# Performance work log

Measured on AMD Instinct MI355X. Metric: run time of the kernel, lower is better.

The kernel has to match this reference:

```python
import jax, jax.numpy as jnp
import numpy as np


def _qkernel(r, i, j, k):
    # Build the real-valued block kernel of a quaternion dense layer.
    # r,i,j,k: [in/4, out/4] -> kernel [in, out] implementing the Hamilton product.
    col_r = jnp.concatenate([r, -i, -j, -k], axis=0)
    col_i = jnp.concatenate([i, r, -k, j], axis=0)
    col_j = jnp.concatenate([j, k, r, -i], axis=0)
    col_k = jnp.concatenate([k, -j, i, r], axis=0)
    return jnp.concatenate([col_r, col_i, col_j, col_k], axis=1)


def setup_inputs() -> dict:
    key = jax.random.key(0)
    ks = jax.random.split(key, 12)
    B, F, H = 32768, 1024, 256
    F4, H4 = F // 4, H // 4
    s_in = 1.0 / np.sqrt(F)
    s_h = 1.0 / np.sqrt(H)
    inp = {
        "x": jax.random.normal(ks[0], (B, F), dtype=jnp.float32),
        "wx_r": jax.random.normal(ks[1], (4, F4, H4), dtype=jnp.float32) * s_in,
        "wx_i": jax.random.normal(ks[2], (4, F4, H4), dtype=jnp.float32) * s_in,
        "wx_j": jax.random.normal(ks[3], (4, F4, H4), dtype=jnp.float32) * s_in,
        "wx_k": jax.random.normal(ks[4], (4, F4, H4), dtype=jnp.float32) * s_in,
        "bx": jnp.zeros((4, H), dtype=jnp.float32),
        "uh_r": jax.random.normal(ks[5], (4, H4, H4), dtype=jnp.float32) * s_h,
        "uh_i": jax.random.normal(ks[6], (4, H4, H4), dtype=jnp.float32) * s_h,
        "uh_j": jax.random.normal(ks[7], (4, H4, H4), dtype=jnp.float32) * s_h,
        "uh_k": jax.random.normal(ks[8], (4, H4, H4), dtype=jnp.float32) * s_h,
        "fco_w": jax.random.normal(ks[9], (H, H), dtype=jnp.float32) * s_h,
        "fco_b": jnp.zeros((H,), dtype=jnp.float32),
    }
    return inp


def reference(x, wx_r, wx_i, wx_j, wx_k, bx, uh_r, uh_i, uh_j, uh_k, fco_w, fco_b):
    # Single-step quaternion LSTM cell with zero initial hidden/cell state.
    # Gate order along leading axis: [forget, input, output, cell].
    Kx = jax.vmap(_qkernel)(wx_r, wx_i, wx_j, wx_k)   # [4, F, H]
    Ku = jax.vmap(_qkernel)(uh_r, uh_i, uh_j, uh_k)   # [4, H, H]
    H = bx.shape[1]
    h0 = jnp.zeros((x.shape[0], H), dtype=x.dtype)
    c0 = h0
    gx = jnp.einsum('bf,gfh->gbh', x, Kx) + bx[:, None, :]   # [4, B, H]
    gu = jnp.einsum('bh,ghk->gbk', h0, Ku)                    # [4, B, H]
    z = gx + gu
    ft = jax.nn.sigmoid(z[0])
    it = jax.nn.sigmoid(z[1])
    ot = jax.nn.sigmoid(z[2])
    at = z[3]
    c = it * jnp.tanh(at) + ft * c0
    h = ot * jnp.tanh(c)
    return h @ fco_w + fco_b
```

## Files before the change

kernel.cpp:

```cpp
#include <hip/hip_runtime.h>
#include <cstdint>
#include <cstddef>

#define WS_WP   0
#define WS_FCO  1572864
#define WS_BP   1703936
#define WS_HVP  1707008

typedef __attribute__((ext_vector_type(8))) __bf16 bf16x8;
typedef __attribute__((ext_vector_type(4))) __bf16 bf16x4;
typedef __attribute__((ext_vector_type(4))) float floatx4;

__device__ __forceinline__ unsigned short f2bf(float f) {
  unsigned int u = __builtin_bit_cast(unsigned int, f);
  u += 0x7fffu + ((u >> 16) & 1u);
  return (unsigned short)(u >> 16);
}

__device__ __forceinline__ float sigmf(float z) {
  return __builtin_amdgcn_rcpf(1.f + __expf(-z));
}
__device__ __forceinline__ float tanh_(float z) {
  return 1.f - 2.f * __builtin_amdgcn_rcpf(1.f + __expf(2.f * z));
}

__device__ __forceinline__ void gld16(const void* g, void* l) {
  __builtin_amdgcn_global_load_lds(
      (const __attribute__((address_space(1))) unsigned int*)g,
      (__attribute__((address_space(3))) unsigned int*)l, 16, 0, 0);
}

__global__ __launch_bounds__(256) void pack_k(
    const float* __restrict__ wr, const float* __restrict__ wi,
    const float* __restrict__ wj, const float* __restrict__ wk,
    const float* __restrict__ bx, const float* __restrict__ fw,
    unsigned short* __restrict__ Wp, unsigned short* __restrict__ Fp,
    float* __restrict__ bp) {
  int t = threadIdx.x;
  if (blockIdx.x < 384) {
    int gpp = blockIdx.x >> 7;
    int oct = blockIdx.x & 127;
    int gp = gpp + 1;
    int h = t;
    int hb = h >> 6, hr = h & 63;
    int f0 = oct << 3;
    int fb = f0 >> 8, fr0 = f0 & 255;
    const int   comp_t[4][4] = {{0,1,2,3},{1,0,3,2},{2,3,0,1},{3,2,1,0}};
    const float sign_t[4][4] = {{1.f,-1.f,-1.f,-1.f},{1.f,1.f,-1.f,1.f},
                                {1.f,1.f,1.f,-1.f},{1.f,-1.f,1.f,1.f}};
    const float* srcs[4] = {wr, wi, wj, wk};
    const float* s = srcs[comp_t[hb][fb]] + ((size_t)((gp << 8) + fr0)) * 64 + hr;
    float sg = sign_t[hb][fb];
    unsigned short v[8];
#pragma unroll
    for (int j = 0; j < 8; ++j) v[j] = f2bf(sg * s[(size_t)j * 64]);
    int c = h * 3 + gpp;
    int cb = c / 192, nl = c % 192;
    int kb = oct >> 2, q = oct & 3;
    int idx16 = (nl << 2) + (q ^ ((nl >> 1) & 3));
    uint4 val = make_uint4(
        (unsigned)v[0] | ((unsigned)v[1] << 16), (unsigned)v[2] | ((unsigned)v[3] << 16),
        (unsigned)v[4] | ((unsigned)v[5] << 16), (unsigned)v[6] | ((unsigned)v[7] << 16));
    *(uint4*)(Wp + (size_t)(cb * 32 + kb) * 6144 + idx16 * 8) = val;
    if (oct == 0) bp[c] = bx[(gp << 8) + h];
  } else {
    int oct = blockIdx.x - 384;
    int n = t;
    int k0 = oct << 3;
    unsigned short v[8];
#pragma unroll
    for (int j = 0; j < 8; ++j) v[j] = f2bf(fw[(size_t)(k0 + j) * 256 + n]);
    int nb = n >> 7, nl = n & 127, kb = oct >> 2, q = oct & 3;
    int idx16 = (nl << 2) + (q ^ ((nl >> 1) & 3));
    uint4 val = make_uint4(
        (unsigned)v[0] | ((unsigned)v[1] << 16), (unsigned)v[2] | ((unsigned)v[3] << 16),
        (unsigned)v[4] | ((unsigned)v[5] << 16), (unsigned)v[6] | ((unsigned)v[7] << 16));
    *(uint4*)(Fp + (size_t)((nb << 3) + kb) * 4096 + idx16 * 8) = val;
  }
}

__global__ __launch_bounds__(512, 4) void gemm1_k(
    const float* __restrict__ x, const unsigned short* __restrict__ Wp,
    const float* __restrict__ bp, unsigned short* __restrict__ hvp) {
  __shared__ char smem[57344];
  float* zep = (float*)smem;

  const int t = threadIdx.x;
  const int lane = t & 63, wid = t >> 6;
  const int wm = wid >> 2, wn = wid & 3;
  const int lrow = lane & 15, q = lane >> 4;
  const int rowt = blockIdx.x;
  const int nbq = blockIdx.y;
  const int cb0 = nbq * 2;
  const int row0 = rowt * 64;
  const float* xbase = x + (size_t)row0 * 1024;

  const int sr = t >> 3, kq = t & 7;
  const int sq8 = kq >> 1, shalf = kq & 1;

  floatx4 acc[2][6];
#pragma unroll
  for (int i = 0; i < 2; ++i)
#pragma unroll
    for (int j = 0; j < 6; ++j) acc[i][j] = (floatx4){0.f, 0.f, 0.f, 0.f};

#define STAGE_B(bufi, kt)                                                     \
  {                                                                           \
    unsigned short* sBs_ = (unsigned short*)(smem + (bufi) * 28672 + 4096);   \
    const unsigned short* bt0_ = Wp + ((size_t)cb0 * 32 + (kt)) * 6144;       \
    _Pragma("unroll")                                                         \
    for (int i_ = 0; i_ < 3; ++i_) {                                          \
      int s_ = t + i_ * 512;                                                  \
      int cbL_ = s_ >= 768;                                                   \
      const unsigned short* src_ =                                            \
          bt0_ + (size_t)cbL_ * 196608 + (s_ - cbL_ * 768) * 8;               \
      gld16(src_, sBs_ + s_ * 8);                                             \
    }                                                                         \
  }
#define LOAD_A(ra, kt)                                                        \
  { ra = *(const float4*)(xbase + (size_t)sr * 1024 + (kt) * 32 + kq * 4); }
#define WRITE_A(ra, bufi)                                                     \
  {                                                                           \
    unsigned short* sAs_ = (unsigned short*)(smem + (bufi) * 28672);          \
    int slot_ = (sr << 2) + (sq8 ^ ((sr >> 1) & 3));                          \
    bf16x4 v_;                                                                \
    v_[0] = (__bf16)ra.x; v_[1] = (__bf16)ra.y;                               \
    v_[2] = (__bf16)ra.z; v_[3] = (__bf16)ra.w;                               \
    *(bf16x4*)(sAs_ + slot_ * 8 + shalf * 4) = v_;                            \
  }
#define COMPUTE(bufi)                                                         \
  {                                                                           \
    const unsigned short* sA_ = (const unsigned short*)(smem + (bufi) * 28672);\
    const unsigned short* sB_ = sA_ + 2048;                                   \
    bf16x8 af[2], bf[6];                                                      \
    _Pragma("unroll")                                                         \
    for (int mt = 0; mt < 2; ++mt) {                                          \
      int m = wm * 32 + mt * 16 + lrow;                                       \
      int slot = (m << 2) + (q ^ ((m >> 1) & 3));                             \
      af[mt] = *(const bf16x8*)(const void*)(sA_ + slot * 8);                 \
    }                                                                         \
    _Pragma("unroll")                                                         \
    for (int nt = 0; nt < 6; ++nt) {                                          \
      int nl = (wn & 1) * 96 + nt * 16 + lrow;                                \
      int off16 = (nl << 2) + (q ^ ((nl >> 1) & 3));                          \
      bf[nt] = *(const bf16x8*)(const void*)(                                 \
          sB_ + ((size_t)(wn >> 1) * 768 + off16) * 8);                       \
    }                                                                         \
    _Pragma("unroll")                                                         \
    for (int mt = 0; mt < 2; ++mt)                                            \
      _Pragma("unroll")                                                       \
      for (int nt = 0; nt < 6; ++nt)                                          \
        acc[mt][nt] = __builtin_amdgcn_mfma_f32_16x16x32_bf16(                \
            af[mt], bf[nt], acc[mt][nt], 0, 0, 0);                            \
  }

  float4 ra;
  LOAD_A(ra, 0)
  STAGE_B(0, 0)
  WRITE_A(ra, 0)
  __syncthreads();

  for (int kt = 0; kt < 32; ++kt) {
    if (kt < 31) {
      LOAD_A(ra, kt + 1)
      STAGE_B((kt + 1) & 1, kt + 1)
    }
    COMPUTE(kt & 1)
    if (kt < 31) WRITE_A(ra, (kt + 1) & 1)
    __syncthreads();
  }
#undef COMPUTE
#undef STAGE_B
#undef LOAD_A
#undef WRITE_A

  const float* bp0 = bp + cb0 * 192;
  const int er = t >> 4, oc = t & 15;
  const int cbL = oc >> 3, oo = oc & 7;
  const int mb128 = rowt >> 1;
#pragma unroll
  for (int pass = 0; pass < 2; ++pass) {
    if (wm == pass) {
#pragma unroll
      for (int mt = 0; mt < 2; ++mt)
#pragma unroll
        for (int nt = 0; nt < 6; ++nt)
#pragma unroll
          for (int r = 0; r < 4; ++r)
            zep[(mt * 16 + q * 4 + r) * 385 + wn * 96 + nt * 16 + lrow] = acc[mt][nt][r];
    }
    __syncthreads();
    {
      int ml = (rowt & 1) * 64 + pass * 32 + er;
      unsigned short v[8];
#pragma unroll
      for (int j = 0; j < 8; ++j) {
        int hl = oo * 8 + j;
        int cz = cbL * 192 + hl * 3;
        float zi = zep[er * 385 + cz + 0] + bp0[cz + 0];
        float zo = zep[er * 385 + cz + 1] + bp0[cz + 1];
        float zc = zep[er * 385 + cz + 2] + bp0[cz + 2];
        float it = sigmf(zi);
        float ot = sigmf(zo);
        float cc = it * tanh_(zc);
        v[j] = f2bf(ot * tanh_(cc));
      }
      int ktile = (cb0 + cbL) * 2 + (oo >> 2), qq = oo & 3;
      int idx16 = (ml << 2) + (qq ^ ((ml >> 1) & 3));
      uint4 val = make_uint4(
          (unsigned)v[0] | ((unsigned)v[1] << 16), (unsigned)v[2] | ((unsigned)v[3] << 16),
          (unsigned)v[4] | ((unsigned)v[5] << 16), (unsigned)v[6] | ((unsigned)v[7] << 16));
      *(uint4*)(hvp + (size_t)(mb128 * 8 + ktile) * 4096 + idx16 * 8) = val;
    }
    __syncthreads();
  }
}

__global__ __launch_bounds__(256, 4) void gemm2_k(
    const unsigned short* __restrict__ hvp, const unsigned short* __restrict__ Fp,
    const float* __restrict__ fcob, float* __restrict__ out) {
  __shared__ unsigned short sB[32768];
  const int t = threadIdx.x;
  const int lane = t & 63, wid = t >> 6;
  const int wm = wid >> 1, wn = wid & 1;
  const int lrow = lane & 15, q = lane >> 4;
  const int mb = blockIdx.x, nb = blockIdx.y;

  const unsigned short* fpb = Fp + (size_t)nb * 32768;
#pragma unroll
  for (int i = 0; i < 16; ++i) gld16(fpb + (t + i * 256) * 8, sB + (t + i * 256) * 8);

  floatx4 acc[4][4];
#pragma unroll
  for (int i = 0; i < 4; ++i)
#pragma unroll
    for (int j = 0; j < 4; ++j) acc[i][j] = (floatx4){0.f, 0.f, 0.f, 0.f};
  __syncthreads();

#pragma unroll
  for (int kt = 0; kt < 8; ++kt) {
    const unsigned short* at_ = hvp + (size_t)(mb * 8 + kt) * 4096;
    bf16x8 af[4], bf[4];
#pragma unroll
    for (int mt = 0; mt < 4; ++mt) {
      int m = wm * 64 + mt * 16 + lrow;
      int o = (m << 2) + (q ^ ((m >> 1) & 3));
      af[mt] = *(const bf16x8*)(const void*)(at_ + o * 8);
    }
#pragma unroll
    for (int nt = 0; nt < 4; ++nt) {
      int n = wn * 64 + nt * 16 + lrow;
      int o = (n << 2) + (q ^ ((n >> 1) & 3));
      bf[nt] = *(const bf16x8*)(const void*)(sB + kt * 4096 + o * 8);
    }
#pragma unroll
    for (int mt = 0; mt < 4; ++mt)
#pragma unroll
      for (int nt = 0; nt < 4; ++nt)
        acc[mt][nt] = __builtin_amdgcn_mfma_f32_16x16x32_bf16(af[mt], bf[nt], acc[mt][nt], 0, 0, 0);
  }
#pragma unroll
  for (int nt = 0; nt < 4; ++nt) {
    int colg = nb * 128 + wn * 64 + nt * 16 + lrow;
    float bias = fcob[colg];
#pragma unroll
    for (int mt = 0; mt < 4; ++mt) {
      int rowg = mb * 128 + wm * 64 + mt * 16 + q * 4;
#pragma unroll
      for (int r = 0; r < 4; ++r)
        out[(size_t)(rowg + r) * 256 + colg] = acc[mt][nt][r] + bias;
    }
  }
}

extern "C" void kernel_launch(void* const* d_in, const int* in_sizes, int n_in,
                              void* d_out, int out_size, void* d_ws, size_t ws_size,
                              hipStream_t stream) {
  const float* x  = (const float*)d_in[0];
  const float* wr = (const float*)d_in[1];
  const float* wi = (const float*)d_in[2];
  const float* wj = (const float*)d_in[3];
  const float* wk = (const float*)d_in[4];
  const float* bx = (const float*)d_in[5];
  const float* fw = (const float*)d_in[10];
  const float* fb = (const float*)d_in[11];
  char* ws = (char*)d_ws;
  unsigned short* Wp  = (unsigned short*)(ws + WS_WP);
  unsigned short* Fp  = (unsigned short*)(ws + WS_FCO);
  float*          bp  = (float*)(ws + WS_BP);
  unsigned short* hvp = (unsigned short*)(ws + WS_HVP);
  float*          out = (float*)d_out;

  hipLaunchKernelGGL(pack_k,  dim3(416),    dim3(256), 0, stream, wr, wi, wj, wk, bx, fw, Wp, Fp, bp);
  hipLaunchKernelGGL(gemm1_k, dim3(512, 2), dim3(512), 0, stream, x, Wp, bp, hvp);
  hipLaunchKernelGGL(gemm2_k, dim3(256, 2), dim3(256), 0, stream, hvp, Fp, fb, out);
}
```

Baseline: 292.0 us.

## Pre-pack x into swizzled bf16 tiles and use async-LDS pipelined GEMM

Adds a pass to the packing kernel that converts the fp32 input x into bf16 tiles with an LDS-friendly swizzle in workspace. A new GEMM kernel streams those tiles with global_load_lds through a 3-stage buffer, using a 128x192 block tile and 256 threads. The aim is to halve GEMM operand bytes and remove in-loop conversion. The cost is an extra full read of x plus a bf16 write and re-read, and the path is used only when the workspace is large enough. Otherwise the old kernel runs.

New measurement: 298.9 us. 1.02x slower.

```diff
diff --git a/kernel.cpp b/kernel.cpp
--- a/kernel.cpp
+++ b/kernel.cpp
@@ -6,6 +6,8 @@
 #define WS_FCO  1572864
 #define WS_BP   1703936
 #define WS_HVP  1707008
+#define WS_XP   18484224
+#define WS_NEED 85593088ull
 
 typedef __attribute__((ext_vector_type(8))) __bf16 bf16x8;
 typedef __attribute__((ext_vector_type(4))) __bf16 bf16x4;
@@ -34,8 +36,9 @@
     const float* __restrict__ wr, const float* __restrict__ wi,
     const float* __restrict__ wj, const float* __restrict__ wk,
     const float* __restrict__ bx, const float* __restrict__ fw,
+    const float* __restrict__ x,
     unsigned short* __restrict__ Wp, unsigned short* __restrict__ Fp,
-    float* __restrict__ bp) {
+    float* __restrict__ bp, unsigned short* __restrict__ xp) {
   int t = threadIdx.x;
   if (blockIdx.x < 384) {
     int gpp = blockIdx.x >> 7;
@@ -63,7 +66,7 @@
         (unsigned)v[4] | ((unsigned)v[5] << 16), (unsigned)v[6] | ((unsigned)v[7] << 16));
     *(uint4*)(Wp + (size_t)(cb * 32 + kb) * 6144 + idx16 * 8) = val;
     if (oct == 0) bp[c] = bx[(gp << 8) + h];
-  } else {
+  } else if (blockIdx.x < 416) {
     int oct = blockIdx.x - 384;
     int n = t;
     int k0 = oct << 3;
@@ -76,10 +79,154 @@
         (unsigned)v[0] | ((unsigned)v[1] << 16), (unsigned)v[2] | ((unsigned)v[3] << 16),
         (unsigned)v[4] | ((unsigned)v[5] << 16), (unsigned)v[6] | ((unsigned)v[7] << 16));
     *(uint4*)(Fp + (size_t)((nb << 3) + kb) * 4096 + idx16 * 8) = val;
-  }
-}
-
-__global__ __launch_bounds__(512, 4) void gemm1_k(
+  } else {
+    int b = blockIdx.x - 416;
+    int mb = b >> 3, kb8 = b & 7;
+    const float* xb = x + (size_t)mb * 128 * 1024 + kb8 * 128;
+    unsigned short* xpb = xp + ((size_t)mb * 32 + (size_t)kb8 * 4) * 4096;
+#pragma unroll
+    for (int i = 0; i < 8; ++i) {
+      int s = t + i * 256;
+      int tile = s >> 9, idx16 = s & 511;
+      int ml = idx16 >> 2;
+      int q = (idx16 & 3) ^ ((ml >> 1) & 3);
+      const float* src = xb + (size_t)ml * 1024 + tile * 32 + q * 8;
+      float4 a0 = *(const float4*)src;
+      float4 a1 = *(const float4*)(src + 4);
+      uint4 val = make_uint4(
+          (unsigned)f2bf(a0.x) | ((unsigned)f2bf(a0.y) << 16),
+          (unsigned)f2bf(a0.z) | ((unsigned)f2bf(a0.w) << 16),
+          (unsigned)f2bf(a1.x) | ((unsigned)f2bf(a1.y) << 16),
+          (unsigned)f2bf(a1.z) | ((unsigned)f2bf(a1.w) << 16));
+      *(uint4*)(xpb + (size_t)tile * 4096 + idx16 * 8) = val;
+    }
+  }
+}
+
+__global__ __launch_bounds__(256, 2) void gemm1_xp_k(
+    const unsigned short* __restrict__ xp, const unsigned short* __restrict__ Wp,
+    const float* __restrict__ bp, unsigned short* __restrict__ hvp) {
+  __shared__ char smem[61440];
+  float* zep = (float*)smem;
+
+  const int t = threadIdx.x;
+  const int lane = t & 63, wid = t >> 6;
+  const int wm = wid >> 1, wn = wid & 1;
+  const int lrow = lane & 15, q = lane >> 4;
+  const int rowt = blockIdx.x;
+  const int cby = blockIdx.y;
+  const unsigned short* apb = xp + (size_t)rowt * 32 * 4096;
+  const unsigned short* wpb = Wp + (size_t)cby * 32 * 6144;
+
+  floatx4 acc[4][6];
+#pragma unroll
+  for (int i = 0; i < 4; ++i)
+#pragma unroll
+    for (int j = 0; j < 6; ++j) acc[i][j] = (floatx4){0.f, 0.f, 0.f, 0.f};
+
+#define STAGE(bufi, kt)                                                       \
+  {                                                                           \
+    char* base_ = smem + (bufi) * 20480;                                      \
+    unsigned short* sA_ = (unsigned short*)base_;                             \
+    unsigned short* sB_ = (unsigned short*)(base_ + 8192);                    \
+    const unsigned short* at_ = apb + (size_t)(kt) * 4096;                    \
+    const unsigned short* bt_ = wpb + (size_t)(kt) * 6144;                    \
+    gld16(at_ + t * 8, sA_ + t * 8);                                          \
+    gld16(at_ + (t + 256) * 8, sA_ + (t + 256) * 8);                          \
+    _Pragma("unroll")                                                         \
+    for (int i_ = 0; i_ < 3; ++i_) {                                          \
+      int s_ = t + i_ * 256;                                                  \
+      gld16(bt_ + s_ * 8, sB_ + s_ * 8);                                      \
+    }                                                                         \
+  }
+#define COMPUTE(bufi)                                                         \
+  {                                                                           \
+    const unsigned short* sA_ = (const unsigned short*)(smem + (bufi) * 20480);\
+    const unsigned short* sB_ = sA_ + 4096;                                   \
+    bf16x8 af[4], bf[6];                                                      \
+    _Pragma("unroll")                                                         \
+    for (int mt = 0; mt < 4; ++mt) {                                          \
+      int m = wm * 64 + mt * 16 + lrow;                                       \
+      int slot = (m << 2) + (q ^ ((m >> 1) & 3));                             \
+      af[mt] = *(const bf16x8*)(const void*)(sA_ + slot * 8);                 \
+    }                                                                         \
+    _Pragma("unroll")                                                         \
+    for (int nt = 0; nt < 6; ++nt) {                                          \
+      int n = wn * 96 + nt * 16 + lrow;                                       \
+      int off16 = (n << 2) + (q ^ ((n >> 1) & 3));                            \
+      bf[nt] = *(const bf16x8*)(const void*)(sB_ + off16 * 8);                \
+    }                                                                         \
+    _Pragma("unroll")                                                         \
+    for (int mt = 0; mt < 4; ++mt)                                            \
+      _Pragma("unroll")                                                       \
+      for (int nt = 0; nt < 6; ++nt)                                          \
+        acc[mt][nt] = __builtin_amdgcn_mfma_f32_16x16x32_bf16(                \
+            af[mt], bf[nt], acc[mt][nt], 0, 0, 0);                            \
+  }
+
+  STAGE(0, 0)
+  STAGE(1, 1)
+  asm volatile("s_waitcnt vmcnt(5)" ::: "memory");
+  __builtin_amdgcn_s_barrier();
+  asm volatile("" ::: "memory");
+
+  for (int kt = 0; kt < 32; ++kt) {
+    if (kt < 30) STAGE((kt + 2) % 3, kt + 2)
+    COMPUTE(kt % 3)
+    if (kt < 30) {
+      asm volatile("s_waitcnt vmcnt(5)" ::: "memory");
+    } else {
+      asm volatile("s_waitcnt vmcnt(0)" ::: "memory");
+    }
+    asm volatile("s_waitcnt lgkmcnt(0)" ::: "memory");
+    __builtin_amdgcn_s_barrier();
+    asm volatile("" ::: "memory");
+  }
+#undef COMPUTE
+#undef STAGE
+  __syncthreads();
+
+  const float* bp0 = bp + cby * 192;
+  const int er = t >> 3, oc = t & 7;
+#pragma unroll
+  for (int pass = 0; pass < 4; ++pass) {
+    if (wm == (pass >> 1)) {
+      int mtb = (pass & 1) * 2;
+#pragma unroll
+      for (int mi = 0; mi < 2; ++mi)
+#pragma unroll
+        for (int nt = 0; nt < 6; ++nt)
+#pragma unroll
+          for (int r = 0; r < 4; ++r)
+            zep[(mi * 16 + q * 4 + r) * 201 + wn * 96 + nt * 16 + lrow] = acc[mtb + mi][nt][r];
+    }
+    __syncthreads();
+    {
+      int ml = pass * 32 + er;
+      unsigned short v[8];
+#pragma unroll
+      for (int j = 0; j < 8; ++j) {
+        int hl = oc * 8 + j;
+        float zi = zep[er * 201 + hl * 3 + 0] + bp0[hl * 3 + 0];
+        float zo = zep[er * 201 + hl * 3 + 1] + bp0[hl * 3 + 1];
+        float zc = zep[er * 201 + hl * 3 + 2] + bp0[hl * 3 + 2];
+        float it = sigmf(zi);
+        float ot = sigmf(zo);
+        float cc = it * tanh_(zc);
+        v[j] = f2bf(ot * tanh_(cc));
+      }
+      int ktile = cby * 2 + (oc >> 2), qq = oc & 3;
+      int idx16 = (ml << 2) + (qq ^ ((ml >> 1) & 3));
+      uint4 val = make_uint4(
+          (unsigned)v[0] | ((unsigned)v[1] << 16), (unsigned)v[2] | ((unsigned)v[3] << 16),
+          (unsigned)v[4] | ((unsigned)v[5] << 16), (unsigned)v[6] | ((unsigned)v[7] << 16));
+      *(uint4*)(hvp + (size_t)(rowt * 8 + ktile) * 4096 + idx16 * 8) = val;
+    }
+    __syncthreads();
+  }
+}
+
+__global__ __launch_bounds__(512, 4) void gemm1_fb_k(
     const float* __restrict__ x, const unsigned short* __restrict__ Wp,
     const float* __restrict__ bp, unsigned short* __restrict__ hvp) {
   __shared__ char smem[57344];
@@ -291,7 +438,15 @@
   unsigned short* hvp = (unsigned short*)(ws + WS_HVP);
   float*          out = (float*)d_out;
 
-  hipLaunchKernelGGL(pack_k,  dim3(416),    dim3(256), 0, stream, wr, wi, wj, wk, bx, fw, Wp, Fp, bp);
-  hipLaunchKernelGGL(gemm1_k, dim3(512, 2), dim3(512), 0, stream, x, Wp, bp, hvp);
+  const bool big = ws_size >= WS_NEED;
+  unsigned short* xp = big ? (unsigned short*)(ws + WS_XP) : hvp;
+
+  hipLaunchKernelGGL(pack_k, dim3(big ? 2464 : 416), dim3(256), 0, stream,
+                     wr, wi, wj, wk, bx, fw, x, Wp, Fp, bp, xp);
+  if (big) {
+    hipLaunchKernelGGL(gemm1_xp_k, dim3(256, 4), dim3(256), 0, stream, xp, Wp, bp, hvp);
+  } else {
+    hipLaunchKernelGGL(gemm1_fb_k, dim3(512, 2), dim3(512), 0, stream, x, Wp, bp, hvp);
+  }
   hipLaunchKernelGGL(gemm2_k, dim3(256, 2), dim3(256), 0, stream, hvp, Fp, fb, out);
 }
```
